# Kernel tuning notes

Hardware: AMD Instinct MI355X
Metric: run time of the kernel (lower is better)

The kernel has to match this reference:

```python
import jax, jax.numpy as jnp
import numpy as np

EMBED_DIM = 1024
NUM_HEADS = 16
HEAD_DIM = EMBED_DIM // NUM_HEADS


def setup_inputs() -> dict:
    key = jax.random.key(0)
    ks = jax.random.split(key, 5)
    B, N = 4, 2048
    s_in = 1.0 / np.sqrt(EMBED_DIM)
    return {
        "x": jax.random.normal(ks[0], (B, N, EMBED_DIM), dtype=jnp.float32),
        "qkv_w": jax.random.uniform(ks[1], (3 * EMBED_DIM, EMBED_DIM), jnp.float32, -s_in, s_in),
        "qkv_b": jax.random.uniform(ks[2], (3 * EMBED_DIM,), jnp.float32, -s_in, s_in),
        "o_w": jax.random.uniform(ks[3], (EMBED_DIM, EMBED_DIM), jnp.float32, -s_in, s_in),
        "o_b": jax.random.uniform(ks[4], (EMBED_DIM,), jnp.float32, -s_in, s_in),
    }


def reference(x, qkv_w, qkv_b, o_w, o_b):
    B, N, E = x.shape
    H, D = NUM_HEADS, HEAD_DIM
    # qkv: [B, N, 3E] -> [B, N, H, 3D] -> [B, H, N, 3D], then chunk last dim
    qkv = (jnp.einsum('bne,fe->bnf', x, qkv_w) + qkv_b)
    qkv = qkv.reshape(B, N, H, 3 * D).transpose(0, 2, 1, 3)
    q, k, v = jnp.split(qkv, 3, axis=-1)
    scale = 1.0 / np.sqrt(D)
    scores = jnp.einsum('bhqd,bhkd->bhqk', q, k) * scale
    attn = jax.nn.softmax(scores, axis=-1)  # dropout is identity in eval mode
    out = jnp.einsum('bhqk,bhkd->bhqd', attn, v)
    out = out.transpose(0, 2, 1, 3).reshape(B, N, E)
    return jnp.einsum('bne,fe->bnf', out, o_w) + o_b
```

## Files before the change

### kernel.cpp

```cpp
#include <hip/hip_runtime.h>

typedef unsigned short u16;
typedef float f32x4 __attribute__((ext_vector_type(4)));
typedef float f32x16 __attribute__((ext_vector_type(16)));
typedef short bf16x8 __attribute__((ext_vector_type(8)));
typedef int i32x2 __attribute__((ext_vector_type(2)));

__device__ __forceinline__ u16 f2bf(float f){
  union { float f; unsigned u; } x; x.f = f;
  unsigned r = (x.u + 0x7FFFu + ((x.u >> 16) & 1u)) >> 16;
  return (u16)r;
}

__device__ __forceinline__ unsigned cvtpk(float lo, float hi){
  unsigned r;
  asm("v_cvt_pk_bf16_f32 %0, %1, %2" : "=v"(r) : "v"(lo), "v"(hi));
  return r;
}

__device__ __forceinline__ void exp4q(float& a, float& b, float& c, float& d){
  asm("v_exp_f32 %0, %0\n\t"
      "v_exp_f32 %1, %1\n\t"
      "v_exp_f32 %2, %2\n\t"
      "v_exp_f32 %3, %3\n\t"
      "s_nop 1"
      : "+v"(a), "+v"(b), "+v"(c), "+v"(d));
}

__device__ __forceinline__ f32x4 mfma_bf16(bf16x8 a, bf16x8 b, f32x4 c){
  return __builtin_amdgcn_mfma_f32_16x16x32_bf16(a, b, c, 0, 0, 0);
}

__device__ __forceinline__ f32x16 mfma32(bf16x8 a, bf16x8 b, f32x16 c){
  return __builtin_amdgcn_mfma_f32_32x32x16_bf16(a, b, c, 0, 0, 0);
}

__device__ __forceinline__ void gload16(const u16* g, u16* l){
  __builtin_amdgcn_global_load_lds((__attribute__((address_space(1))) void*)g,
                                   (__attribute__((address_space(3))) void*)l, 16, 0, 0);
}

__global__ void cvt_bf16(const float* __restrict__ in, u16* __restrict__ out, int n4){
  int stride = gridDim.x * blockDim.x;
  for (int i = blockIdx.x*blockDim.x + threadIdx.x; i < n4; i += stride){
    float4 v = ((const float4*)in)[i];
    ushort4 o;
    o.x = f2bf(v.x); o.y = f2bf(v.y); o.z = f2bf(v.z); o.w = f2bf(v.w);
    ((ushort4*)out)[i] = o;
  }
}

template<int NCH, int NTHR>
__device__ __forceinline__ void stage32(const u16* src, int ld, u16* lds, int tid){
#pragma unroll
  for (int i = 0; i < NCH/NTHR; i++){
    int c = i*NTHR + tid;
    int row = c >> 2, slot = c & 3;
    int col = ((slot ^ (row & 3)) << 3);
    gload16(src + (size_t)row*ld + col, lds + ((size_t)(c & ~63) << 3));
  }
}

template<int NTHR>
__device__ __forceinline__ void stage64(const u16* src, int ld, u16* lds, int tid){
#pragma unroll
  for (int i = 0; i < 512/NTHR; i++){
    int c = i*NTHR + tid;
    int row = c >> 3, slot = c & 7;
    int col = ((slot ^ (row & 7)) << 3);
    gload16(src + (size_t)row*ld + col, lds + ((size_t)(c & ~63) << 3));
  }
}

__launch_bounds__(256)
__global__ void gemm_bt1(const u16* __restrict__ A, const u16* __restrict__ Bw,
                         const float* __restrict__ bias, float* __restrict__ Co,
                         int M, int Nf, int K)
{
  __shared__ u16 lsA[2][128*32];
  __shared__ u16 lsB[2][128*32];
  int tid = threadIdx.x;
  int wave = tid >> 6, lane = tid & 63, grp = lane >> 4, l16 = lane & 15;
  int ntn = Nf >> 7;
  int bm = blockIdx.x / ntn, bn = blockIdx.x % ntn;
  const u16* Ab = A + (size_t)bm*128*K;
  const u16* Bb = Bw + (size_t)bn*128*K;
  int wm = wave >> 1, wn = wave & 1;
  f32x4 acc[4][4] = {};

  stage32<512,256>(Ab, K, lsA[0], tid);
  stage32<512,256>(Bb, K, lsB[0], tid);
  int nk = K >> 5;
  for (int t = 0; t < nk; t++){
    __syncthreads();
    int cur = t & 1;
    if (t + 1 < nk){
      stage32<512,256>(Ab + ((t+1) << 5), K, lsA[cur^1], tid);
      stage32<512,256>(Bb + ((t+1) << 5), K, lsB[cur^1], tid);
    }
    const u16* la = lsA[cur];
    const u16* lb = lsB[cur];
    bf16x8 af[4], bfr[4];
#pragma unroll
    for (int mf = 0; mf < 4; mf++){
      int row = wm*64 + mf*16 + l16;
      af[mf] = *(const bf16x8*)(la + row*32 + ((grp ^ (row & 3)) << 3));
    }
#pragma unroll
    for (int nf = 0; nf < 4; nf++){
      int row = wn*64 + nf*16 + l16;
      bfr[nf] = *(const bf16x8*)(lb + row*32 + ((grp ^ (row & 3)) << 3));
    }
#pragma unroll
    for (int mf = 0; mf < 4; mf++)
#pragma unroll
      for (int nf = 0; nf < 4; nf++)
        acc[mf][nf] = mfma_bf16(af[mf], bfr[nf], acc[mf][nf]);
  }

  int mrow0 = bm*128 + wm*64;
  int f0 = bn*128 + wn*64;
#pragma unroll
  for (int nf = 0; nf < 4; nf++){
    int f = f0 + nf*16 + l16;
    float bv = bias[f];
#pragma unroll
    for (int mf = 0; mf < 4; mf++){
      int mbase = mrow0 + mf*16 + grp*4;
#pragma unroll
      for (int r = 0; r < 4; r++)
        Co[(size_t)(mbase + r)*Nf + f] = acc[mf][nf][r] + bv;
    }
  }
}

__launch_bounds__(512, 1)
__global__ void gemm_qkv(const u16* __restrict__ A, const u16* __restrict__ Bw,
                         const float* __restrict__ bias,
                         u16* __restrict__ Qp, u16* __restrict__ Kp,
                         u16* __restrict__ Vt, int M, int Nf, int K)
{
  __shared__ u16 lsA[2][256*64];
  __shared__ u16 lsB[2][256*64];
  int tid = threadIdx.x;
  int lane = tid & 63, grp = lane >> 4, l16 = lane & 15;
  int wave = tid >> 6;
  int wr = wave >> 2, wc = wave & 3;
  int ntn = Nf >> 8;
  int bid = (blockIdx.x & 7) * 48 + (blockIdx.x >> 3);
  int bm = bid / ntn, bn = bid % ntn;
  const u16* Ab = A + (size_t)bm*256*K;
  const u16* Bb = Bw + (size_t)bn*256*K;

  f32x4 acc[8][4] = {};

  auto stageHalf = [&](const u16* src, u16* lds, int h){
#pragma unroll
    for (int i = 0; i < 2; i++){
      int c = i*512 + tid;
      int row = h*128 + (c >> 3);
      int col = (((c & 7) ^ (row & 7)) << 3);
      gload16(src + (size_t)row*K + col, lds + h*8192 + ((size_t)(c & ~63) << 3));
    }
  };

  stageHalf(Ab, lsA[0], 0);
  stageHalf(Bb, lsB[0], 0);
  stageHalf(Ab, lsA[0], 1);
  stageHalf(Bb, lsB[0], 1);
  asm volatile("s_waitcnt vmcnt(4)" ::: "memory");

  int nkt = K >> 6;
  for (int t = 0; t < nkt; t++){
    const u16* la = lsA[t & 1];
    const u16* lb = lsB[t & 1];
    const u16* As = Ab + ((t+1) << 6);
    const u16* Bs = Bb + ((t+1) << 6);
    u16* dA = lsA[(t+1) & 1];
    u16* dB = lsB[(t+1) & 1];
    bool pf = (t + 1) < nkt;
    bf16x8 af[4][2], bf[2][2];

    __builtin_amdgcn_s_barrier();
#pragma unroll
    for (int m = 0; m < 4; m++){
      int grow = (m*2 + wr)*16 + l16;
#pragma unroll
      for (int ks = 0; ks < 2; ks++)
        af[m][ks] = *(const bf16x8*)(la + grow*64 + (((ks*4+grp) ^ (grow & 7)) << 3));
    }
#pragma unroll
    for (int n = 0; n < 2; n++){
      int brow = (n*4 + wc)*16 + l16;
#pragma unroll
      for (int ks = 0; ks < 2; ks++)
        bf[n][ks] = *(const bf16x8*)(lb + brow*64 + (((ks*4+grp) ^ (brow & 7)) << 3));
    }
    if (pf) stageHalf(As, dA, 0);
    __builtin_amdgcn_s_setprio(1);
#pragma unroll
    for (int m = 0; m < 4; m++)
#pragma unroll
      for (int n = 0; n < 2; n++)
#pragma unroll
        for (int ks = 0; ks < 2; ks++)
          acc[m][n] = mfma_bf16(af[m][ks], bf[n][ks], acc[m][n]);
    __builtin_amdgcn_s_setprio(0);
    if (pf) asm volatile("s_waitcnt vmcnt(4)" ::: "memory");
    else    asm volatile("s_waitcnt vmcnt(2)" ::: "memory");

    __builtin_amdgcn_s_barrier();
#pragma unroll
    for (int m = 0; m < 4; m++){
      int grow = ((m+4)*2 + wr)*16 + l16;
#pragma unroll
      for (int ks = 0; ks < 2; ks++)
        af[m][ks] = *(const bf16x8*)(la + grow*64 + (((ks*4+grp) ^ (grow & 7)) << 3));
    }
    if (pf) stageHalf(Bs, dB, 0);
    __builtin_amdgcn_s_setprio(1);
#pragma unroll
    for (int m = 0; m < 4; m++)
#pragma unroll
      for (int n = 0; n < 2; n++)
#pragma unroll
        for (int ks = 0; ks < 2; ks++)
          acc[m+4][n] = mfma_bf16(af[m][ks], bf[n][ks], acc[m+4][n]);
    __builtin_amdgcn_s_setprio(0);
    if (pf) asm volatile("s_waitcnt vmcnt(4)" ::: "memory");
    else    asm volatile("s_waitcnt vmcnt(0)" ::: "memory");

    __builtin_amdgcn_s_barrier();
#pragma unroll
    for (int n = 0; n < 2; n++){
      int brow = ((n+2)*4 + wc)*16 + l16;
#pragma unroll
      for (int ks = 0; ks < 2; ks++)
        bf[n][ks] = *(const bf16x8*)(lb + brow*64 + (((ks*4+grp) ^ (brow & 7)) << 3));
    }
    if (pf) stageHalf(As, dA, 1);
    __builtin_amdgcn_s_setprio(1);
#pragma unroll
    for (int m = 0; m < 4; m++)
#pragma unroll
      for (int n = 0; n < 2; n++)
#pragma unroll
        for (int ks = 0; ks < 2; ks++)
          acc[m+4][n+2] = mfma_bf16(af[m][ks], bf[n][ks], acc[m+4][n+2]);
    __builtin_amdgcn_s_setprio(0);

#pragma unroll
    for (int m = 0; m < 4; m++){
      int grow = (m*2 + wr)*16 + l16;
#pragma unroll
      for (int ks = 0; ks < 2; ks++)
        af[m][ks] = *(const bf16x8*)(la + grow*64 + (((ks*4+grp) ^ (grow & 7)) << 3));
    }
    if (pf) stageHalf(Bs, dB, 1);
    __builtin_amdgcn_s_setprio(1);
#pragma unroll
    for (int m = 0; m < 4; m++)
#pragma unroll
      for (int n = 0; n < 2; n++)
#pragma unroll
        for (int ks = 0; ks < 2; ks++)
          acc[m][n+2] = mfma_bf16(af[m][ks], bf[n][ks], acc[m][n+2]);
    __builtin_amdgcn_s_setprio(0);
    if (pf) asm volatile("s_waitcnt vmcnt(4)" ::: "memory");
  }

#pragma unroll
  for (int n = 0; n < 4; n++){
    int f = bn*256 + (n*4 + wc)*16 + l16;
    float bv = bias[f];
    int h = f / 192, c = f % 192;
#pragma unroll
    for (int m = 0; m < 8; m++){
      int mbase = bm*256 + (m*2 + wr)*16 + grp*4;
      int bb = mbase >> 11, n0 = mbase & 2047;
      size_t bh = (size_t)bb*16 + h;
      if (c >= 128){
        ushort4 w;
        w.x = f2bf(acc[m][n][0] + bv);
        w.y = f2bf(acc[m][n][1] + bv);
        w.z = f2bf(acc[m][n][2] + bv);
        w.w = f2bf(acc[m][n][3] + bv);
        *(ushort4*)(Vt + (bh*64 + (size_t)(c - 128))*2048 + n0) = w;
      } else {
        u16* dst = (c < 64) ? Qp : Kp;
        float sc = (c < 64) ? 0.18033688011f : 1.0f;
        int cc = c & 63;
#pragma unroll
        for (int r = 0; r < 4; r++)
          dst[(bh*2048 + n0 + r)*64 + cc] = f2bf((acc[m][n][r] + bv) * sc);
      }
    }
  }
}

__device__ __forceinline__ bf16x8 packP(const f32x16& pp, int base){
  unsigned t0 = cvtpk(pp[base+0], pp[base+1]);
  unsigned t1 = cvtpk(pp[base+2], pp[base+3]);
  unsigned t2 = cvtpk(pp[base+4], pp[base+5]);
  unsigned t3 = cvtpk(pp[base+6], pp[base+7]);
  i32x2 r02 = __builtin_amdgcn_permlane32_swap((int)t0, (int)t2, false, false);
  i32x2 r13 = __builtin_amdgcn_permlane32_swap((int)t1, (int)t3, false, false);
  union { unsigned u[4]; bf16x8 v; } pu;
  pu.u[0] = (unsigned)r02.x;
  pu.u[1] = (unsigned)r13.x;
  pu.u[2] = (unsigned)r02.y;
  pu.u[3] = (unsigned)r13.y;
  return pu.v;
}

__device__ __forceinline__ void expv16(f32x16& p){
#pragma unroll
  for (int r = 0; r < 16; r += 4){
    float a = p[r], b = p[r+1], c = p[r+2], d = p[r+3];
    exp4q(a, b, c, d);
    p[r] = a; p[r+1] = b; p[r+2] = c; p[r+3] = d;
  }
}

__launch_bounds__(512, 4)
__global__ void attn_fwd(const u16* __restrict__ Qg, const u16* __restrict__ Kg,
                         const u16* __restrict__ Vtg, u16* __restrict__ Oa)
{
  __shared__ u16 kl[4][64*64];
  __shared__ u16 vl[4][64*64];
  int tid = threadIdx.x;
  int lane = tid & 63, wave = tid >> 6;
  int q32 = lane & 31, hi = lane >> 5;
  int bid = (blockIdx.x & 7) * 64 + (blockIdx.x >> 3);
  int bh = bid >> 3, qt = bid & 7;
  int b = bh >> 4, h = bh & 15;
  int q0 = qt*256 + wave*32;
  const u16* Qb = Qg + ((size_t)bh*2048 + q0)*64;
  const u16* Kb = Kg + (size_t)bh*2048*64;
  const u16* Vb = Vtg + (size_t)bh*64*2048;

  bf16x8 qf[4];
#pragma unroll
  for (int s = 0; s < 4; s++)
    qf[s] = *(const bf16x8*)(Qb + q32*64 + s*16 + hi*8);

  f32x16 lacc = {};
  f32x16 oacc[2] = {};

#pragma unroll
  for (int t = 0; t < 3; t++){
    stage64<512>(Kb + (size_t)t*64*64, 64, kl[t], tid);
    stage64<512>(Vb + t*64, 2048, vl[t], tid);
  }

  for (int kt = 0; kt < 32; kt++){
    if (kt < 30)       asm volatile("s_waitcnt vmcnt(4)" ::: "memory");
    else if (kt == 30) asm volatile("s_waitcnt vmcnt(2)" ::: "memory");
    else               asm volatile("s_waitcnt vmcnt(0)" ::: "memory");
    __builtin_amdgcn_s_barrier();
    __builtin_amdgcn_sched_barrier(0);
    if (kt + 3 < 32){
      stage64<512>(Kb + (size_t)(kt+3)*64*64, 64, kl[(kt+3)&3], tid);
      stage64<512>(Vb + (kt+3)*64, 2048, vl[(kt+3)&3], tid);
    }
    const u16* lk = kl[kt & 3];
    const u16* lv = vl[kt & 3];

    f32x16 p0 = {}, p1 = {};
    __builtin_amdgcn_s_setprio(1);
#pragma unroll
    for (int s = 0; s < 4; s++){
      int r0 = q32;
      bf16x8 k0 = *(const bf16x8*)(lk + r0*64 + (((s*2+hi) ^ (r0 & 7)) << 3));
      p0 = mfma32(k0, qf[s], p0);
      int r1 = 32 + q32;
      bf16x8 k1 = *(const bf16x8*)(lk + r1*64 + (((s*2+hi) ^ (r1 & 7)) << 3));
      p1 = mfma32(k1, qf[s], p1);
    }
    __builtin_amdgcn_s_setprio(0);

    expv16(p0); expv16(p1);
#pragma unroll
    for (int r = 0; r < 16; r++) lacc[r] += p0[r];
#pragma unroll
    for (int r = 0; r < 16; r++) lacc[r] += p1[r];

#pragma unroll
    for (int ks = 0; ks < 4; ks++){
      bf16x8 pb = packP((ks < 2) ? p0 : p1, (ks & 1) * 8);
      __builtin_amdgcn_s_setprio(1);
      int rowd0 = q32;
      bf16x8 v0 = *(const bf16x8*)(lv + rowd0*64 + (((ks*2+hi) ^ (rowd0 & 7)) << 3));
      oacc[0] = mfma32(v0, pb, oacc[0]);
      int rowd1 = 32 + q32;
      bf16x8 v1 = *(const bf16x8*)(lv + rowd1*64 + (((ks*2+hi) ^ (rowd1 & 7)) << 3));
      oacc[1] = mfma32(v1, pb, oacc[1]);
      __builtin_amdgcn_s_setprio(0);
    }
  }

#pragma unroll
  for (int r = 0; r < 8; r++) lacc[r] += lacc[r+8];
#pragma unroll
  for (int r = 0; r < 4; r++) lacc[r] += lacc[r+4];
  float l = (lacc[0] + lacc[1]) + (lacc[2] + lacc[3]);
  l += __shfl_xor(l, 32, 64);
  float inv = 1.0f / l;

  size_t obase = ((size_t)b*2048 + q0 + q32)*1024 + h*64;
#pragma unroll
  for (int dblk = 0; dblk < 2; dblk++)
#pragma unroll
    for (int rb = 0; rb < 4; rb++){
      ushort4 w;
      w.x = f2bf(oacc[dblk][rb*4+0] * inv);
      w.y = f2bf(oacc[dblk][rb*4+1] * inv);
      w.z = f2bf(oacc[dblk][rb*4+2] * inv);
      w.w = f2bf(oacc[dblk][rb*4+3] * inv);
      *(ushort4*)(Oa + obase + dblk*32 + rb*8 + hi*4) = w;
    }
}

extern "C" void kernel_launch(void* const* d_in, const int* in_sizes, int n_in,
                              void* d_out, int out_size, void* d_ws, size_t ws_size,
                              hipStream_t stream)
{
  const float* x    = (const float*)d_in[0];
  const float* qkvw = (const float*)d_in[1];
  const float* qkvb = (const float*)d_in[2];
  const float* ow   = (const float*)d_in[3];
  const float* ob   = (const float*)d_in[4];
  float* out = (float*)d_out;

  u16* xb = (u16*)d_ws;
  u16* wq = xb + (size_t)8192*1024;
  u16* wo = wq + (size_t)3072*1024;
  u16* Qp = wo + (size_t)1024*1024;
  u16* Kp = Qp + (size_t)64*2048*64;
  u16* Vt = Kp + (size_t)64*2048*64;
  u16* Oa = Vt + (size_t)64*2048*64;

  cvt_bf16<<<1024, 256, 0, stream>>>(x, xb, (8192*1024)/4);
  cvt_bf16<<<512, 256, 0, stream>>>(qkvw, wq, (3072*1024)/4);
  cvt_bf16<<<256, 256, 0, stream>>>(ow, wo, (1024*1024)/4);

  gemm_qkv<<<32*12, 512, 0, stream>>>(xb, wq, qkvb, Qp, Kp, Vt, 8192, 3072, 1024);
  attn_fwd<<<512, 512, 0, stream>>>(Qp, Kp, Vt, Oa);
  gemm_bt1<<<64*8, 256, 0, stream>>>(Oa, wo, ob, out, 8192, 1024, 1024);
}
```

Baseline: 193.6 us.

## Drop LDS staging in attention, read K/V from global; merge convert kernels

The attention kernel no longer stages K and V tiles into shared memory through an asynchronous multi-buffered pipeline with barriers. Each wave now loads its K and V fragments directly from global memory and relies on the cache, using 256-thread blocks and twice as many blocks. The three fp32-to-bf16 conversion launches are merged into one kernel to save launch overhead. The V reads are strided by 2048 elements per row and every wave refetches the same K/V data, which risks more cache and global traffic and exposed load latency now that nothing is prefetched.

```diff
diff --git a/kernel.cpp b/kernel.cpp
--- a/kernel.cpp
+++ b/kernel.cpp
@@ -40,13 +40,21 @@
                                    (__attribute__((address_space(3))) void*)l, 16, 0, 0);
 }
 
-__global__ void cvt_bf16(const float* __restrict__ in, u16* __restrict__ out, int n4){
+__global__ void cvt_all(const float* __restrict__ x, const float* __restrict__ w1,
+                        const float* __restrict__ w2,
+                        u16* __restrict__ ox, u16* __restrict__ o1, u16* __restrict__ o2,
+                        int nx4, int n14, int n24){
   int stride = gridDim.x * blockDim.x;
-  for (int i = blockIdx.x*blockDim.x + threadIdx.x; i < n4; i += stride){
-    float4 v = ((const float4*)in)[i];
+  int ntot = nx4 + n14 + n24;
+  for (int i = blockIdx.x*blockDim.x + threadIdx.x; i < ntot; i += stride){
+    const float* src; u16* dst; int j = i;
+    if (j < nx4){ src = x; dst = ox; }
+    else if (j < nx4 + n14){ j -= nx4; src = w1; dst = o1; }
+    else { j -= nx4 + n14; src = w2; dst = o2; }
+    float4 v = ((const float4*)src)[j];
     ushort4 o;
     o.x = f2bf(v.x); o.y = f2bf(v.y); o.z = f2bf(v.z); o.w = f2bf(v.w);
-    ((ushort4*)out)[i] = o;
+    ((ushort4*)dst)[j] = o;
   }
 }
 
@@ -57,17 +65,6 @@
     int c = i*NTHR + tid;
     int row = c >> 2, slot = c & 3;
     int col = ((slot ^ (row & 3)) << 3);
-    gload16(src + (size_t)row*ld + col, lds + ((size_t)(c & ~63) << 3));
-  }
-}
-
-template<int NTHR>
-__device__ __forceinline__ void stage64(const u16* src, int ld, u16* lds, int tid){
-#pragma unroll
-  for (int i = 0; i < 512/NTHR; i++){
-    int c = i*NTHR + tid;
-    int row = c >> 3, slot = c & 7;
-    int col = ((slot ^ (row & 7)) << 3);
     gload16(src + (size_t)row*ld + col, lds + ((size_t)(c & ~63) << 3));
   }
 }
@@ -322,19 +319,17 @@
   }
 }
 
-__launch_bounds__(512, 4)
+__launch_bounds__(256)
 __global__ void attn_fwd(const u16* __restrict__ Qg, const u16* __restrict__ Kg,
                          const u16* __restrict__ Vtg, u16* __restrict__ Oa)
 {
-  __shared__ u16 kl[4][64*64];
-  __shared__ u16 vl[4][64*64];
   int tid = threadIdx.x;
   int lane = tid & 63, wave = tid >> 6;
   int q32 = lane & 31, hi = lane >> 5;
-  int bid = (blockIdx.x & 7) * 64 + (blockIdx.x >> 3);
-  int bh = bid >> 3, qt = bid & 7;
+  int bid = (blockIdx.x & 7) * 128 + (blockIdx.x >> 3);
+  int bh = bid >> 4, qt = bid & 15;
   int b = bh >> 4, h = bh & 15;
-  int q0 = qt*256 + wave*32;
+  int q0 = qt*128 + wave*32;
   const u16* Qb = Qg + ((size_t)bh*2048 + q0)*64;
   const u16* Kb = Kg + (size_t)bh*2048*64;
   const u16* Vb = Vtg + (size_t)bh*64*2048;
@@ -347,34 +342,17 @@
   f32x16 lacc = {};
   f32x16 oacc[2] = {};
 
-#pragma unroll
-  for (int t = 0; t < 3; t++){
-    stage64<512>(Kb + (size_t)t*64*64, 64, kl[t], tid);
-    stage64<512>(Vb + t*64, 2048, vl[t], tid);
-  }
-
   for (int kt = 0; kt < 32; kt++){
-    if (kt < 30)       asm volatile("s_waitcnt vmcnt(4)" ::: "memory");
-    else if (kt == 30) asm volatile("s_waitcnt vmcnt(2)" ::: "memory");
-    else               asm volatile("s_waitcnt vmcnt(0)" ::: "memory");
-    __builtin_amdgcn_s_barrier();
-    __builtin_amdgcn_sched_barrier(0);
-    if (kt + 3 < 32){
-      stage64<512>(Kb + (size_t)(kt+3)*64*64, 64, kl[(kt+3)&3], tid);
-      stage64<512>(Vb + (kt+3)*64, 2048, vl[(kt+3)&3], tid);
-    }
-    const u16* lk = kl[kt & 3];
-    const u16* lv = vl[kt & 3];
+    const u16* kbase = Kb + (size_t)kt*64*64;
+    const u16* vbase = Vb + kt*64;
 
     f32x16 p0 = {}, p1 = {};
     __builtin_amdgcn_s_setprio(1);
 #pragma unroll
     for (int s = 0; s < 4; s++){
-      int r0 = q32;
-      bf16x8 k0 = *(const bf16x8*)(lk + r0*64 + (((s*2+hi) ^ (r0 & 7)) << 3));
+      bf16x8 k0 = *(const bf16x8*)(kbase + q32*64 + s*16 + hi*8);
       p0 = mfma32(k0, qf[s], p0);
-      int r1 = 32 + q32;
-      bf16x8 k1 = *(const bf16x8*)(lk + r1*64 + (((s*2+hi) ^ (r1 & 7)) << 3));
+      bf16x8 k1 = *(const bf16x8*)(kbase + (32+q32)*64 + s*16 + hi*8);
       p1 = mfma32(k1, qf[s], p1);
     }
     __builtin_amdgcn_s_setprio(0);
@@ -389,11 +367,9 @@
     for (int ks = 0; ks < 4; ks++){
       bf16x8 pb = packP((ks < 2) ? p0 : p1, (ks & 1) * 8);
       __builtin_amdgcn_s_setprio(1);
-      int rowd0 = q32;
-      bf16x8 v0 = *(const bf16x8*)(lv + rowd0*64 + (((ks*2+hi) ^ (rowd0 & 7)) << 3));
+      bf16x8 v0 = *(const bf16x8*)(vbase + (size_t)q32*2048 + ks*16 + hi*8);
       oacc[0] = mfma32(v0, pb, oacc[0]);
-      int rowd1 = 32 + q32;
-      bf16x8 v1 = *(const bf16x8*)(lv + rowd1*64 + (((ks*2+hi) ^ (rowd1 & 7)) << 3));
+      bf16x8 v1 = *(const bf16x8*)(vbase + (size_t)(32+q32)*2048 + ks*16 + hi*8);
       oacc[1] = mfma32(v1, pb, oacc[1]);
       __builtin_amdgcn_s_setprio(0);
     }
@@ -440,11 +416,10 @@
   u16* Vt = Kp + (size_t)64*2048*64;
   u16* Oa = Vt + (size_t)64*2048*64;
 
-  cvt_bf16<<<1024, 256, 0, stream>>>(x, xb, (8192*1024)/4);
-  cvt_bf16<<<512, 256, 0, stream>>>(qkvw, wq, (3072*1024)/4);
-  cvt_bf16<<<256, 256, 0, stream>>>(ow, wo, (1024*1024)/4);
+  cvt_all<<<2048, 256, 0, stream>>>(x, qkvw, ow, xb, wq, wo,
+                                    (8192*1024)/4, (3072*1024)/4, (1024*1024)/4);
 
   gemm_qkv<<<32*12, 512, 0, stream>>>(xb, wq, qkvb, Qp, Kp, Vt, 8192, 3072, 1024);
-  attn_fwd<<<512, 512, 0, stream>>>(Qp, Kp, Vt, Oa);
+  attn_fwd<<<1024, 256, 0, stream>>>(Qp, Kp, Vt, Oa);
   gemm_bt1<<<64*8, 256, 0, stream>>>(Oa, wo, ob, out, 8192, 1024, 1024);
 }
```

Result: slower. 376.9 us (+94.7%).
